# Performance work log

Measured on AMD Instinct MI355X. Metric: run time of the kernel, lower is better.

Reference implementation:

```python
import jax, jax.numpy as jnp
import numpy as np

B, C, H, W = 16, 256, 64, 64


def setup_inputs() -> dict:
    key = jax.random.key(0)
    kx, ky, kz, kw, kb, kg = jax.random.split(key, 6)
    x = jax.random.normal(kx, (B, C, H, W), dtype=jnp.float32)
    y = jax.random.normal(ky, (B, C, H, W), dtype=jnp.float32)
    z = jax.random.normal(kz, (B, C, H, W), dtype=jnp.float32)
    # 1x1 conv params (stored as [out_c, in_c]); gamma is a learned scalar
    # (init 0 in the module; use a nonzero value so the output exercises the path)
    conv_w = jax.random.normal(kw, (C, C), dtype=jnp.float32) / np.sqrt(C)
    conv_b = jax.random.normal(kb, (C,), dtype=jnp.float32) * 0.01
    gamma = jax.random.normal(kg, (1,), dtype=jnp.float32) * 0.1
    return {"x": x, "y": y, "z": z, "conv_w": conv_w, "conv_b": conv_b, "gamma": gamma}


def _channel_attn(q, k_src):
    # q: [B, C, N]; k_src: [B, C, H, W] -> energy [B, C, C]
    b, c, n = q.shape
    k = k_src.reshape(b, c, n)
    energy = jnp.einsum('bcn,bdn->bcd', q, k)
    # reversed-max trick: max - energy, then softmax over last dim
    energy_new = jnp.max(energy, axis=-1, keepdims=True) - energy
    return jax.nn.softmax(energy_new, axis=-1)


def reference(x, y, z, conv_w, conv_b, gamma):
    b, c, h, w = x.shape
    q = x.reshape(b, c, h * w)  # query == key1 == value
    # three attention maps share query and value; sum before the value bmm
    attn = _channel_attn(q, x) + _channel_attn(q, y) + _channel_attn(q, z)
    out = jnp.einsum('bcd,bdn->bcn', attn, q).reshape(b, c, h, w)
    # 1x1 conv == per-pixel channel mixing
    out = jnp.einsum('oc,bchw->bohw', conv_w, out) + conv_b[None, :, None, None]
    return gamma * out + x
```

## Files before the change

### kernel.cpp

```cpp
#include <hip/hip_runtime.h>
#include <hip/hip_bf16.h>


#define B_ 16
#define C_ 256
#define N_ 4096
#define KSPLIT 4
#define KCHUNK (N_ / KSPLIT)

#define MODE_BF16 0
#define MODE_F32  1

typedef __bf16 bf16_t;
typedef bf16_t bf16x8 __attribute__((ext_vector_type(8)));
typedef float  f32x4  __attribute__((ext_vector_type(4)));

#define MFMA(a, b, c) __builtin_amdgcn_mfma_f32_16x16x32_bf16(a, b, c, 0, 0, 0)

__device__ int    g_mode;
__device__ bf16_t g_q[(size_t)B_ * C_ * N_];
__device__ bf16_t g_qT[(size_t)B_ * N_ * C_];
__device__ bf16_t g_cw[C_ * C_];
__device__ float  g_cb[C_];
__device__ float  g_gamma;
__device__ float  g_Ep[(size_t)KSPLIT * 3 * B_ * C_ * C_];
__device__ bf16_t g_attnT[(size_t)B_ * C_ * C_];
__device__ bf16_t g_M[(size_t)B_ * C_ * C_];
__device__ bf16_t g_P[(size_t)B_ * C_ * N_];

__global__ __launch_bounds__(256) void setup_kernel(
    const float* __restrict__ xf, const void* __restrict__ cw,
    const void* __restrict__ cb, const void* __restrict__ gm)
{
  __shared__ unsigned red[256];
  const int t = threadIdx.x;
  unsigned m = 0;
  for (int i = t; i < 4096; i += 256)
    m = max(m, __float_as_uint(xf[i]) & 0x7fffffffu);
  red[t] = m;
  __syncthreads();
  for (int s = 128; s > 0; s >>= 1) {
    if (t < s) red[t] = max(red[t], red[t + s]);
    __syncthreads();
  }
  const int mode = (red[0] > 0x44800000u) ? MODE_BF16 : MODE_F32;
  if (t == 0) g_mode = mode;

  if (mode == MODE_F32) {
    for (int i = t * 8; i < C_ * C_; i += 256 * 8) {
      const float* s = (const float*)cw + i;
      float4 a = *(const float4*)s;
      float4 b = *(const float4*)(s + 4);
      bf16x8 v;
      v[0] = (bf16_t)a.x; v[1] = (bf16_t)a.y; v[2] = (bf16_t)a.z; v[3] = (bf16_t)a.w;
      v[4] = (bf16_t)b.x; v[5] = (bf16_t)b.y; v[6] = (bf16_t)b.z; v[7] = (bf16_t)b.w;
      *(bf16x8*)(g_cw + i) = v;
    }
    if (t < C_) g_cb[t] = ((const float*)cb)[t];
    if (t == 0) g_gamma = ((const float*)gm)[0];
  } else {
    for (int i = t * 8; i < C_ * C_; i += 256 * 8)
      *(bf16x8*)(g_cw + i) = *(const bf16x8*)((const bf16_t*)cw + i);
    if (t < C_) g_cb[t] = (float)((const bf16_t*)cb)[t];
    if (t == 0) g_gamma = (float)((const bf16_t*)gm)[0];
  }
}

__global__ __launch_bounds__(256) void convert_xT(const void* __restrict__ x)
{
  __shared__ bf16_t Ts[64][64];
  const int t  = threadIdx.x;
  const int r  = t >> 3;
  const int nb = t & 7;
  const int co = nb * 8;
  const int n0 = blockIdx.x * 64;
  const int c0 = blockIdx.y * 64;
  const int b  = blockIdx.z;
  const size_t base = (size_t)b * C_ * N_;
  const int mode = g_mode;

  bf16x8 v[2];
  if (mode == MODE_F32) {
#pragma unroll
    for (int p = 0; p < 2; ++p) {
      const float* s = (const float*)x + base + (size_t)(c0 + r + p * 32) * N_ + n0 + co;
      float4 a = *(const float4*)s;
      float4 b4 = *(const float4*)(s + 4);
      bf16x8 w;
      w[0] = (bf16_t)a.x; w[1] = (bf16_t)a.y; w[2] = (bf16_t)a.z; w[3] = (bf16_t)a.w;
      w[4] = (bf16_t)b4.x; w[5] = (bf16_t)b4.y; w[6] = (bf16_t)b4.z; w[7] = (bf16_t)b4.w;
      v[p] = w;
    }
  } else {
#pragma unroll
    for (int p = 0; p < 2; ++p)
      v[p] = *(const bf16x8*)((const bf16_t*)x + base + (size_t)(c0 + r + p * 32) * N_ + n0 + co);
  }

#pragma unroll
  for (int p = 0; p < 2; ++p) {
    const int cl = r + p * 32;
    if (mode == MODE_F32)
      *(bf16x8*)(g_q + base + (size_t)(c0 + cl) * N_ + n0 + co) = v[p];
    const int swz = nb ^ ((cl >> 3) & 7);
    *(bf16x8*)(&Ts[cl][swz * 8]) = v[p];
  }
  __syncthreads();

#pragma unroll
  for (int p = 0; p < 2; ++p) {
    const int nl = r + p * 32;
    bf16x8 w;
#pragma unroll
    for (int j = 0; j < 8; ++j) {
      const int c = co + j;
      const int k = (c >> 3) & 7;
      w[j] = Ts[c][(((nl >> 3) ^ k) * 8) + (nl & 7)];
    }
    *(bf16x8*)(g_qT + (size_t)b * N_ * C_ + (size_t)(n0 + nl) * C_ + c0 + co) = w;
  }
}

__global__ __launch_bounds__(256) void energy_kernel(
    const void* __restrict__ xraw, const void* __restrict__ yraw,
    const void* __restrict__ zraw)
{
  const int tile = blockIdx.x & 3;
  const int kc   = blockIdx.x >> 2;
  const int s    = blockIdx.y;
  const int b    = blockIdx.z;

  const int mode = g_mode;
  const bf16_t* q =
      (mode == MODE_BF16 ? (const bf16_t*)xraw : g_q) + (size_t)b * C_ * N_;

  const bf16_t* kb16 = nullptr;
  const float*  kf32 = nullptr;
  if (s == 0) {
    kb16 = q;
  } else if (mode == MODE_BF16) {
    kb16 = (const bf16_t*)(s == 1 ? yraw : zraw) + (size_t)b * C_ * N_;
  } else {
    kf32 = (const float*)(s == 1 ? yraw : zraw) + (size_t)b * C_ * N_;
  }

  const int tile_m = (tile & 1) * 128;
  const int tile_d = (tile >> 1) * 128;

  __shared__ bf16_t As[128][72];
  __shared__ bf16_t Bs[128][72];

  const int tid  = threadIdx.x;
  const int w    = tid >> 6;
  const int lane = tid & 63;
  const int wm   = (w & 1) * 64;
  const int wd   = (w >> 1) * 64;
  const int lrow = lane & 15;
  const int lk   = (lane >> 4) * 8;

  const int srow = tid >> 3;
  const int soff = (tid & 7) * 8;

  f32x4 acc[4][4] = {};

  const int kbeg = kc * KCHUNK;
  for (int k0 = kbeg; k0 < kbeg + KCHUNK; k0 += 64) {
    bf16x8 av[4], bv[4];
#pragma unroll
    for (int i = 0; i < 4; ++i) {
      int r = srow + i * 32;
      av[i] = *(const bf16x8*)(q + (size_t)(tile_m + r) * N_ + k0 + soff);
    }
    if (kf32) {
#pragma unroll
      for (int i = 0; i < 4; ++i) {
        int r = srow + i * 32;
        const float* sp = kf32 + (size_t)(tile_d + r) * N_ + k0 + soff;
        float4 a = *(const float4*)sp;
        float4 c = *(const float4*)(sp + 4);
        bf16x8 v;
        v[0] = (bf16_t)a.x; v[1] = (bf16_t)a.y; v[2] = (bf16_t)a.z; v[3] = (bf16_t)a.w;
        v[4] = (bf16_t)c.x; v[5] = (bf16_t)c.y; v[6] = (bf16_t)c.z; v[7] = (bf16_t)c.w;
        bv[i] = v;
      }
    } else {
#pragma unroll
      for (int i = 0; i < 4; ++i) {
        int r = srow + i * 32;
        bv[i] = *(const bf16x8*)(kb16 + (size_t)(tile_d + r) * N_ + k0 + soff);
      }
    }
    __syncthreads();
#pragma unroll
    for (int i = 0; i < 4; ++i) {
      int r = srow + i * 32;
      *(bf16x8*)(&As[r][soff]) = av[i];
      *(bf16x8*)(&Bs[r][soff]) = bv[i];
    }
    __syncthreads();
#pragma unroll
    for (int kk = 0; kk < 64; kk += 32) {
      bf16x8 af[4], bfr[4];
#pragma unroll
      for (int i = 0; i < 4; ++i)
        af[i] = *(const bf16x8*)(&As[wm + i * 16 + lrow][kk + lk]);
#pragma unroll
      for (int j = 0; j < 4; ++j)
        bfr[j] = *(const bf16x8*)(&Bs[wd + j * 16 + lrow][kk + lk]);
#pragma unroll
      for (int i = 0; i < 4; ++i)
#pragma unroll
        for (int j = 0; j < 4; ++j)
          acc[i][j] = MFMA(af[i], bfr[j], acc[i][j]);
    }
  }

  float* Eb = g_Ep + (((size_t)kc * 3 + s) * B_ + b) * (size_t)C_ * C_;
  const int orow0 = tile_m + wm + (lane >> 4) * 4;
  const int ocol0 = tile_d + wd + (lane & 15);
#pragma unroll
  for (int i = 0; i < 4; ++i)
#pragma unroll
    for (int j = 0; j < 4; ++j)
#pragma unroll
      for (int r = 0; r < 4; ++r)
        Eb[(size_t)(orow0 + i * 16 + r) * C_ + (ocol0 + j * 16)] = acc[i][j][r];
}

__global__ __launch_bounds__(256) void softmax_kernel()
{
  const int b    = blockIdx.y;
  const int c    = blockIdx.x * 4 + (threadIdx.x >> 6);
  const int lane = threadIdx.x & 63;
  const int d0   = lane * 4;

  float a0 = 0.f, a1 = 0.f, a2 = 0.f, a3 = 0.f;
#pragma unroll
  for (int s = 0; s < 3; ++s) {
    float e0 = 0.f, e1 = 0.f, e2 = 0.f, e3 = 0.f;
#pragma unroll
    for (int kc = 0; kc < KSPLIT; ++kc) {
      const float4 ep = *(const float4*)(
          g_Ep + ((((size_t)kc * 3 + s) * B_ + b) * C_ + c) * (size_t)C_ + d0);
      e0 += ep.x; e1 += ep.y; e2 += ep.z; e3 += ep.w;
    }
    float mn = fminf(fminf(e0, e1), fminf(e2, e3));
#pragma unroll
    for (int m = 32; m > 0; m >>= 1) mn = fminf(mn, __shfl_xor(mn, m));
    const float p0 = __expf(mn - e0);
    const float p1 = __expf(mn - e1);
    const float p2 = __expf(mn - e2);
    const float p3 = __expf(mn - e3);
    float Z = p0 + p1 + p2 + p3;
#pragma unroll
    for (int m = 32; m > 0; m >>= 1) Z += __shfl_xor(Z, m);
    const float rZ = 1.0f / Z;
    a0 += p0 * rZ; a1 += p1 * rZ; a2 += p2 * rZ; a3 += p3 * rZ;
  }
  bf16_t* At = g_attnT + (size_t)b * C_ * C_;
  At[(size_t)(d0 + 0) * C_ + c] = (bf16_t)a0;
  At[(size_t)(d0 + 1) * C_ + c] = (bf16_t)a1;
  At[(size_t)(d0 + 2) * C_ + c] = (bf16_t)a2;
  At[(size_t)(d0 + 3) * C_ + c] = (bf16_t)a3;
}

__global__ __launch_bounds__(256) void mconv_kernel()
{
  const int tile = blockIdx.x;
  const int b    = blockIdx.y;
  const int tile_o = (tile & 3) * 64;
  const int tile_d = (tile >> 2) * 64;
  const int tid  = threadIdx.x;
  const int w    = tid >> 6;
  const int lane = tid & 63;
  const int wo   = (w & 1) * 32;
  const int wd   = (w >> 1) * 32;
  const int lrow = lane & 15;
  const int lk   = (lane >> 4) * 8;

  const bf16_t* At = g_attnT + (size_t)b * C_ * C_;
  f32x4 acc[2][2] = {};

  for (int c0 = 0; c0 < C_; c0 += 32) {
    bf16x8 af[2], bfr[2];
#pragma unroll
    for (int i = 0; i < 2; ++i)
      af[i] = *(const bf16x8*)(g_cw + (size_t)(tile_o + wo + i * 16 + lrow) * C_ + c0 + lk);
#pragma unroll
    for (int j = 0; j < 2; ++j)
      bfr[j] = *(const bf16x8*)(At + (size_t)(tile_d + wd + j * 16 + lrow) * C_ + c0 + lk);
#pragma unroll
    for (int i = 0; i < 2; ++i)
#pragma unroll
      for (int j = 0; j < 2; ++j)
        acc[i][j] = MFMA(af[i], bfr[j], acc[i][j]);
  }

  bf16_t* Mb = g_M + (size_t)b * C_ * C_;
  const int orow0 = tile_o + wo + (lane >> 4) * 4;
  const int ocol0 = tile_d + wd + (lane & 15);
#pragma unroll
  for (int i = 0; i < 2; ++i)
#pragma unroll
    for (int j = 0; j < 2; ++j)
#pragma unroll
      for (int r = 0; r < 2 * 2; ++r)
        Mb[(size_t)(orow0 + i * 16 + r) * C_ + (ocol0 + j * 16)] = (bf16_t)acc[i][j][r];
}

__global__ __launch_bounds__(256) void pmq_kernel()
{
  const int tile_n = blockIdx.x * 128;
  const int tile_o = blockIdx.y * 128;
  const int b      = blockIdx.z;

  const bf16_t* Mb = g_M  + (size_t)b * C_ * C_;
  const bf16_t* Qt = g_qT + (size_t)b * N_ * C_;

  __shared__ bf16_t As[128][72];
  __shared__ bf16_t Bs[128][72];

  const int tid  = threadIdx.x;
  const int w    = tid >> 6;
  const int lane = tid & 63;
  const int wo   = (w & 1) * 64;
  const int wn   = (w >> 1) * 64;
  const int lrow = lane & 15;
  const int lk   = (lane >> 4) * 8;

  const int srow = tid >> 3;
  const int soff = (tid & 7) * 8;

  f32x4 acc[4][4] = {};

  for (int d0 = 0; d0 < C_; d0 += 64) {
    bf16x8 av[4], bv[4];
#pragma unroll
    for (int i = 0; i < 4; ++i) {
      int r = srow + i * 32;
      av[i] = *(const bf16x8*)(Mb + (size_t)(tile_o + r) * C_ + d0 + soff);
      bv[i] = *(const bf16x8*)(Qt + (size_t)(tile_n + r) * C_ + d0 + soff);
    }
    __syncthreads();
#pragma unroll
    for (int i = 0; i < 4; ++i) {
      int r = srow + i * 32;
      *(bf16x8*)(&As[r][soff]) = av[i];
      *(bf16x8*)(&Bs[r][soff]) = bv[i];
    }
    __syncthreads();
#pragma unroll
    for (int kk = 0; kk < 64; kk += 32) {
      bf16x8 af[4], bfr[4];
#pragma unroll
      for (int i = 0; i < 4; ++i)
        af[i] = *(const bf16x8*)(&As[wo + i * 16 + lrow][kk + lk]);
#pragma unroll
      for (int j = 0; j < 4; ++j)
        bfr[j] = *(const bf16x8*)(&Bs[wn + j * 16 + lrow][kk + lk]);
#pragma unroll
      for (int i = 0; i < 4; ++i)
#pragma unroll
        for (int j = 0; j < 4; ++j)
          acc[i][j] = MFMA(af[i], bfr[j], acc[i][j]);
    }
  }

  bf16_t* Pb = g_P + (size_t)b * C_ * N_;
  const int orow0 = tile_o + wo + (lane >> 4) * 4;
  const int ocol0 = tile_n + wn + (lane & 15);
#pragma unroll
  for (int i = 0; i < 4; ++i)
#pragma unroll
    for (int j = 0; j < 4; ++j)
#pragma unroll
      for (int r = 0; r < 4; ++r)
        Pb[(size_t)(orow0 + i * 16 + r) * N_ + (ocol0 + j * 16)] = (bf16_t)acc[i][j][r];
}

__global__ __launch_bounds__(256) void epilogue_kernel(
    const void* __restrict__ xraw, void* __restrict__ outraw)
{
  const int row  = blockIdx.x;
  const int o    = row & (C_ - 1);
  const size_t roff = (size_t)row * N_ + (size_t)threadIdx.x * 16;

  const float g    = g_gamma;
  const float bias = g_cb[o];

  const bf16x8 p0 = *(const bf16x8*)(g_P + roff);
  const bf16x8 p1 = *(const bf16x8*)(g_P + roff + 8);
  float v[16];
#pragma unroll
  for (int k = 0; k < 8; ++k) {
    v[k]     = g * ((float)p0[k] + bias);
    v[8 + k] = g * ((float)p1[k] + bias);
  }

  if (g_mode == MODE_F32) {
    const float* xp = (const float*)xraw + roff;
    float*       op = (float*)outraw + roff;
#pragma unroll
    for (int q4 = 0; q4 < 4; ++q4) {
      float4 xv = *(const float4*)(xp + q4 * 4);
      float4 ov;
      ov.x = v[q4 * 4 + 0] + xv.x;
      ov.y = v[q4 * 4 + 1] + xv.y;
      ov.z = v[q4 * 4 + 2] + xv.z;
      ov.w = v[q4 * 4 + 3] + xv.w;
      *(float4*)(op + q4 * 4) = ov;
    }
  } else {
    const bf16_t* xp = (const bf16_t*)xraw + roff;
    bf16_t*       op = (bf16_t*)outraw + roff;
#pragma unroll
    for (int p = 0; p < 2; ++p) {
      bf16x8 xv = *(const bf16x8*)(xp + p * 8);
      bf16x8 ov;
#pragma unroll
      for (int k = 0; k < 8; ++k)
        ov[k] = (bf16_t)(v[p * 8 + k] + (float)xv[k]);
      *(bf16x8*)(op + p * 8) = ov;
    }
  }
}

extern "C" void kernel_launch(void* const* d_in, const int* in_sizes, int n_in,
                              void* d_out, int out_size, void* d_ws, size_t ws_size,
                              hipStream_t stream)
{
  const void* x  = d_in[0];
  const void* y  = d_in[1];
  const void* z  = d_in[2];
  const void* cw = d_in[3];
  const void* cb = d_in[4];
  const void* gm = d_in[5];
  (void)d_ws; (void)ws_size;

  setup_kernel    <<<1,                       256, 0, stream>>>((const float*)x, cw, cb, gm);
  convert_xT      <<<dim3(N_ / 64, C_ / 64, B_), 256, 0, stream>>>(x);
  energy_kernel   <<<dim3(4 * KSPLIT, 3, B_), 256, 0, stream>>>(x, y, z);
  softmax_kernel  <<<dim3(C_ / 4, B_),        256, 0, stream>>>();
  mconv_kernel    <<<dim3(16, B_),            256, 0, stream>>>();
  pmq_kernel      <<<dim3(N_ / 128, 2, B_),   256, 0, stream>>>();
  epilogue_kernel <<<dim3(B_ * C_),           256, 0, stream>>>(x, d_out);
}
```

Baseline: 374.2 us.

## Fuse epilogue into P·Q GEMM and swizzle block order across XCDs

The separate epilogue kernel is folded into the final GEMM. Each block stages its bf16 output tile in shared memory, reusing the A/B staging buffers, then applies bias, gamma and the residual add and writes the final output directly. This removes the global P buffer write and re-read plus one launch. Both the energy and pmq grids are flattened to 1D with a swizzle intended to group blocks of the same batch on the same XCD for L2 locality. The cost is an extra shared-memory pass and additional syncthreads in the GEMM kernel.

New measurement: 356.7 us. 4.7% less time.

```diff
diff --git a/kernel.cpp b/kernel.cpp
--- a/kernel.cpp
+++ b/kernel.cpp
@@ -26,7 +26,6 @@
 __device__ float  g_Ep[(size_t)KSPLIT * 3 * B_ * C_ * C_];
 __device__ bf16_t g_attnT[(size_t)B_ * C_ * C_];
 __device__ bf16_t g_M[(size_t)B_ * C_ * C_];
-__device__ bf16_t g_P[(size_t)B_ * C_ * N_];
 
 __global__ __launch_bounds__(256) void setup_kernel(
     const float* __restrict__ xf, const void* __restrict__ cw,
@@ -125,10 +124,12 @@
     const void* __restrict__ xraw, const void* __restrict__ yraw,
     const void* __restrict__ zraw)
 {
-  const int tile = blockIdx.x & 3;
-  const int kc   = blockIdx.x >> 2;
-  const int s    = blockIdx.y;
-  const int b    = blockIdx.z;
+  const int id   = blockIdx.x;
+  const int swz  = (id & 7) * 96 + (id >> 3);
+  const int tile = swz & 3;
+  const int s    = (swz >> 2) % 3;
+  const int kc   = (swz / 12) & 3;
+  const int b    = swz / 48;
 
   const int mode = g_mode;
   const bf16_t* q =
@@ -304,21 +305,27 @@
 #pragma unroll
     for (int j = 0; j < 2; ++j)
 #pragma unroll
-      for (int r = 0; r < 2 * 2; ++r)
+      for (int r = 0; r < 4; ++r)
         Mb[(size_t)(orow0 + i * 16 + r) * C_ + (ocol0 + j * 16)] = (bf16_t)acc[i][j][r];
 }
 
-__global__ __launch_bounds__(256) void pmq_kernel()
-{
-  const int tile_n = blockIdx.x * 128;
-  const int tile_o = blockIdx.y * 128;
-  const int b      = blockIdx.z;
+__global__ __launch_bounds__(256) void pmq_kernel(
+    const void* __restrict__ xraw, void* __restrict__ outraw)
+{
+  extern __shared__ char smraw[];
+  bf16_t* sm = (bf16_t*)smraw;
+  bf16_t (*As)[72]  = (bf16_t(*)[72])sm;
+  bf16_t (*Bs)[72]  = (bf16_t(*)[72])(sm + 128 * 72);
+  bf16_t (*Os)[136] = (bf16_t(*)[136])sm;
+
+  const int id  = blockIdx.x;
+  const int swz = (id & 7) * 128 + (id >> 3);
+  const int tile_o = (swz & 1) * 128;
+  const int tile_n = ((swz >> 1) & 31) * 128;
+  const int b      = swz >> 6;
 
   const bf16_t* Mb = g_M  + (size_t)b * C_ * C_;
   const bf16_t* Qt = g_qT + (size_t)b * N_ * C_;
-
-  __shared__ bf16_t As[128][72];
-  __shared__ bf16_t Bs[128][72];
 
   const int tid  = threadIdx.x;
   const int w    = tid >> 6;
@@ -366,61 +373,53 @@
     }
   }
 
-  bf16_t* Pb = g_P + (size_t)b * C_ * N_;
-  const int orow0 = tile_o + wo + (lane >> 4) * 4;
-  const int ocol0 = tile_n + wn + (lane & 15);
+  __syncthreads();
+
+  const int orow0 = wo + (lane >> 4) * 4;
+  const int ocol0 = wn + (lane & 15);
 #pragma unroll
   for (int i = 0; i < 4; ++i)
 #pragma unroll
     for (int j = 0; j < 4; ++j)
 #pragma unroll
       for (int r = 0; r < 4; ++r)
-        Pb[(size_t)(orow0 + i * 16 + r) * N_ + (ocol0 + j * 16)] = (bf16_t)acc[i][j][r];
-}
-
-__global__ __launch_bounds__(256) void epilogue_kernel(
-    const void* __restrict__ xraw, void* __restrict__ outraw)
-{
-  const int row  = blockIdx.x;
-  const int o    = row & (C_ - 1);
-  const size_t roff = (size_t)row * N_ + (size_t)threadIdx.x * 16;
-
-  const float g    = g_gamma;
-  const float bias = g_cb[o];
-
-  const bf16x8 p0 = *(const bf16x8*)(g_P + roff);
-  const bf16x8 p1 = *(const bf16x8*)(g_P + roff + 8);
-  float v[16];
-#pragma unroll
-  for (int k = 0; k < 8; ++k) {
-    v[k]     = g * ((float)p0[k] + bias);
-    v[8 + k] = g * ((float)p1[k] + bias);
-  }
-
-  if (g_mode == MODE_F32) {
-    const float* xp = (const float*)xraw + roff;
-    float*       op = (float*)outraw + roff;
-#pragma unroll
-    for (int q4 = 0; q4 < 4; ++q4) {
-      float4 xv = *(const float4*)(xp + q4 * 4);
-      float4 ov;
-      ov.x = v[q4 * 4 + 0] + xv.x;
-      ov.y = v[q4 * 4 + 1] + xv.y;
-      ov.z = v[q4 * 4 + 2] + xv.z;
-      ov.w = v[q4 * 4 + 3] + xv.w;
-      *(float4*)(op + q4 * 4) = ov;
-    }
-  } else {
-    const bf16_t* xp = (const bf16_t*)xraw + roff;
-    bf16_t*       op = (bf16_t*)outraw + roff;
-#pragma unroll
-    for (int p = 0; p < 2; ++p) {
-      bf16x8 xv = *(const bf16x8*)(xp + p * 8);
+        Os[orow0 + i * 16 + r][ocol0 + j * 16] = (bf16_t)acc[i][j][r];
+  __syncthreads();
+
+  const float g   = g_gamma;
+  const int mode  = g_mode;
+  const int rr    = tid >> 4;
+  const int cc    = (tid & 15) * 8;
+  const size_t gbase = (size_t)b * C_ * N_;
+
+#pragma unroll
+  for (int p = 0; p < 8; ++p) {
+    const int r = p * 16 + rr;
+    const float bias = g_cb[tile_o + r];
+    const bf16x8 sv = *(const bf16x8*)(&Os[r][cc]);
+    const size_t off = gbase + (size_t)(tile_o + r) * N_ + tile_n + cc;
+    if (mode == MODE_F32) {
+      const float* xp = (const float*)xraw + off;
+      float*       op = (float*)outraw + off;
+#pragma unroll
+      for (int q4 = 0; q4 < 2; ++q4) {
+        float4 xv = *(const float4*)(xp + q4 * 4);
+        float4 ov;
+        ov.x = g * ((float)sv[q4 * 4 + 0] + bias) + xv.x;
+        ov.y = g * ((float)sv[q4 * 4 + 1] + bias) + xv.y;
+        ov.z = g * ((float)sv[q4 * 4 + 2] + bias) + xv.z;
+        ov.w = g * ((float)sv[q4 * 4 + 3] + bias) + xv.w;
+        *(float4*)(op + q4 * 4) = ov;
+      }
+    } else {
+      const bf16_t* xp = (const bf16_t*)xraw + off;
+      bf16_t*       op = (bf16_t*)outraw + off;
+      const bf16x8 xv = *(const bf16x8*)xp;
       bf16x8 ov;
 #pragma unroll
       for (int k = 0; k < 8; ++k)
-        ov[k] = (bf16_t)(v[p * 8 + k] + (float)xv[k]);
-      *(bf16x8*)(op + p * 8) = ov;
+        ov[k] = (bf16_t)(g * ((float)sv[k] + bias) + (float)xv[k]);
+      *(bf16x8*)op = ov;
     }
   }
 }
@@ -437,11 +436,10 @@
   const void* gm = d_in[5];
   (void)d_ws; (void)ws_size;
 
-  setup_kernel    <<<1,                       256, 0, stream>>>((const float*)x, cw, cb, gm);
-  convert_xT      <<<dim3(N_ / 64, C_ / 64, B_), 256, 0, stream>>>(x);
-  energy_kernel   <<<dim3(4 * KSPLIT, 3, B_), 256, 0, stream>>>(x, y, z);
-  softmax_kernel  <<<dim3(C_ / 4, B_),        256, 0, stream>>>();
-  mconv_kernel    <<<dim3(16, B_),            256, 0, stream>>>();
-  pmq_kernel      <<<dim3(N_ / 128, 2, B_),   256, 0, stream>>>();
-  epilogue_kernel <<<dim3(B_ * C_),           256, 0, stream>>>(x, d_out);
-}
+  setup_kernel   <<<1,                          256, 0, stream>>>((const float*)x, cw, cb, gm);
+  convert_xT     <<<dim3(N_ / 64, C_ / 64, B_), 256, 0, stream>>>(x);
+  energy_kernel  <<<dim3(4 * KSPLIT * 3 * B_),  256, 0, stream>>>(x, y, z);
+  softmax_kernel <<<dim3(C_ / 4, B_),           256, 0, stream>>>();
+  mconv_kernel   <<<dim3(16, B_),               256, 0, stream>>>();
+  pmq_kernel     <<<dim3(N_ / 128 * 2 * B_),    256, 36864, stream>>>(x, d_out);
+}
```
